# Kernel tuning notes

Measured on AMD Instinct MI355X. Metric: run time of the kernel, lower is better.

## Reference

```python
import jax, jax.numpy as jnp
import numpy as np
from jax import lax
from jax.scipy.special import logsumexp

N, M, K = 50000, 1024, 64          # points, nodes, points-per-patch
D_PT, D_NODE = 64, 256             # point / node feature dims
NUM_CORR = 256                     # coarse correspondences (OT batch)
FINE_TOPK = 3
CONF_TH = 0.05
OUT_CORR = 1024                    # fixed-size fine correspondence output
OT_ITERS = 100
NEG = -1e4                         # finite stand-in for -inf (grad-safe)
EPS = 1e-8


def setup_inputs() -> dict:
    key = jax.random.key(0)
    k = jax.random.split(key, 13)
    f = jnp.float32
    return {
        "src_points": jax.random.uniform(k[0], (N, 3), f) * 10.0,
        "tgt_points": jax.random.uniform(k[1], (N, 3), f) * 10.0,
        "src_point_feats": jax.random.normal(k[2], (N, D_PT), f),
        "tgt_point_feats": jax.random.normal(k[3], (N, D_PT), f),
        "src_node_feats": jax.random.normal(k[4], (M, D_NODE), f),
        "tgt_node_feats": jax.random.normal(k[5], (M, D_NODE), f),
        "src_node_xyz": jax.random.uniform(k[6], (M, 3), f) * 10.0,
        "tgt_node_xyz": jax.random.uniform(k[7], (M, 3), f) * 10.0,
        "coarse_w": jax.random.normal(k[8], (D_NODE, D_NODE), f) / np.sqrt(D_NODE),
        "coarse_b": jnp.zeros((D_NODE,), f),
        "fine_w": jax.random.normal(k[9], (D_NODE, D_PT), f) / np.sqrt(D_PT),
        "fine_b": jnp.zeros((D_NODE,), f),
        "alpha": jnp.ones((), f),
    }


def sq_dist(a, b):
    # squared pairwise distance via gram trick, (Na, Nb)
    return (jnp.sum(a * a, -1)[:, None] + jnp.sum(b * b, -1)[None, :]
            - 2.0 * a @ b.T)


def point_to_node_partition(points, nodes):
    d = sq_dist(points, nodes)                       # (N, M)
    p2n = jnp.argmin(d, axis=1)                      # nearest node per point
    m = nodes.shape[0]
    node_masks = jnp.zeros((m,), bool).at[p2n].set(True)
    match = p2n[:, None] == jnp.arange(m)[None, :]   # point assigned to node
    dm = jnp.where(match, d, 1e12)
    _, knn_idx = lax.top_k(-dm.T, K)                 # (M, K) nearest assigned pts
    knn_node = p2n[knn_idx]
    knn_masks = knn_node == jnp.arange(m)[:, None]
    knn_idx = jnp.where(knn_masks, knn_idx, points.shape[0])  # pad index = N
    return node_masks, knn_idx, knn_masks


def coarse_matching(tgt_feats, src_feats, tgt_masks, src_masks):
    # exp(-||.||^2) similarity + dual normalization (GeoTransformer style)
    scores = jnp.exp(-sq_dist(tgt_feats, src_feats))
    valid = tgt_masks[:, None] & src_masks[None, :]
    scores = jnp.where(valid, scores, 0.0)
    s = (scores / (scores.sum(1, keepdims=True) + EPS)) * \
        (scores / (scores.sum(0, keepdims=True) + EPS))
    vals, idx = lax.top_k(s.reshape(-1), NUM_CORR)
    tgt_idx = idx // src_feats.shape[0]
    src_idx = idx % src_feats.shape[0]
    return tgt_idx, src_idx, vals


def log_optimal_transport(scores, row_masks, col_masks, alpha):
    B, R, C = scores.shape
    pad_c = jnp.broadcast_to(alpha, (B, R, 1)).astype(scores.dtype)
    pad_r = jnp.broadcast_to(alpha, (B, 1, C + 1)).astype(scores.dtype)
    padded = jnp.concatenate([jnp.concatenate([scores, pad_c], 2), pad_r], 1)
    inv_r = jnp.concatenate([~row_masks, jnp.zeros((B, 1), bool)], 1)  # (B,R+1)
    inv_c = jnp.concatenate([~col_masks, jnp.zeros((B, 1), bool)], 1)  # (B,C+1)
    padded = jnp.where(inv_r[:, :, None] | inv_c[:, None, :], NEG, padded)
    nr = row_masks.sum(1).astype(scores.dtype)
    nc = col_masks.sum(1).astype(scores.dtype)
    norm = -jnp.log(nr + nc)
    log_mu = jnp.concatenate(
        [jnp.broadcast_to(norm[:, None], (B, R)), (jnp.log(nc) + norm)[:, None]], 1)
    log_mu = jnp.where(inv_r, NEG, log_mu)
    log_nu = jnp.concatenate(
        [jnp.broadcast_to(norm[:, None], (B, C)), (jnp.log(nr) + norm)[:, None]], 1)
    log_nu = jnp.where(inv_c, NEG, log_nu)

    def body(_, uv):
        u, v = uv
        u = log_mu - logsumexp(padded + v[:, None, :], axis=2)
        v = log_nu - logsumexp(padded + u[:, :, None], axis=1)
        return (u, v)

    u, v = lax.fori_loop(0, OT_ITERS, body,
                         (jnp.zeros_like(log_mu), jnp.zeros_like(log_nu)))
    return padded + u[:, :, None] + v[:, None, :] - norm[:, None, None]


def _topk_row_mask(s, k):
    # boolean mask: True where s is among top-k along the last axis
    idx = lax.top_k(s, k)[1]                          # (B, R, k)
    B, R, _ = s.shape
    b = jnp.arange(B)[:, None, None]
    r = jnp.arange(R)[None, :, None]
    return jnp.zeros(s.shape, bool).at[b, r, idx].set(True)


def fine_matching(tgt_knn_pts, src_knn_pts, tgt_masks, src_masks, ot_scores):
    s = jnp.exp(ot_scores[:, :K, :K])                 # drop dustbin
    mask = tgt_masks[:, :, None] & src_masks[:, None, :]
    rm = _topk_row_mask(s, FINE_TOPK)
    cm = jnp.swapaxes(_topk_row_mask(jnp.swapaxes(s, 1, 2), FINE_TOPK), 1, 2)
    corr = rm & cm & (s > CONF_TH) & mask             # mutual topk + threshold
    sm = jnp.where(corr, s, 0.0)
    vals, idx = lax.top_k(sm.reshape(-1), OUT_CORR)   # fixed-size extraction
    b = idx // (K * K)
    r = (idx // K) % K
    c = idx % K
    valid = vals > 0.0
    tp = jnp.where(valid[:, None], tgt_knn_pts[b, r], 0.0)
    sp = jnp.where(valid[:, None], src_knn_pts[b, c], 0.0)
    return tp, sp, jnp.where(valid, vals, 0.0)


def reference(src_points, tgt_points, src_point_feats, tgt_point_feats,
              src_node_feats, tgt_node_feats, src_node_xyz, tgt_node_xyz,
              coarse_w, coarse_b, fine_w, fine_b, alpha):
    def l2n(x):
        return x / jnp.linalg.norm(x, axis=1, keepdims=True)

    s_node_f = l2n(src_node_feats @ coarse_w.T + coarse_b)
    t_node_f = l2n(tgt_node_feats @ coarse_w.T + coarse_b)
    s_pt_f = src_point_feats @ fine_w.T + fine_b       # (N, 256)
    t_pt_f = tgt_point_feats @ fine_w.T + fine_b

    s_nm, s_knn_i, s_knn_m = point_to_node_partition(src_points, src_node_xyz)
    t_nm, t_knn_i, t_knn_m = point_to_node_partition(tgt_points, tgt_node_xyz)

    s_pad_pts = jnp.concatenate([src_points, jnp.zeros((1, 3), src_points.dtype)], 0)
    t_pad_pts = jnp.concatenate([tgt_points, jnp.zeros((1, 3), tgt_points.dtype)], 0)
    s_knn_pts = s_pad_pts[s_knn_i]                     # (M, K, 3)
    t_knn_pts = t_pad_pts[t_knn_i]

    # coarse matching is under no_grad in the original
    t_ci, s_ci, node_scores = coarse_matching(
        lax.stop_gradient(t_node_f), lax.stop_gradient(s_node_f), t_nm, s_nm)

    s_c_knn_i = s_knn_i[s_ci]; t_c_knn_i = t_knn_i[t_ci]     # (B, K)
    s_c_knn_m = s_knn_m[s_ci]; t_c_knn_m = t_knn_m[t_ci]
    s_c_knn_p = s_knn_pts[s_ci]; t_c_knn_p = t_knn_pts[t_ci]  # (B, K, 3)

    s_pad_f = jnp.concatenate([s_pt_f, jnp.zeros((1, D_NODE), s_pt_f.dtype)], 0)
    t_pad_f = jnp.concatenate([t_pt_f, jnp.zeros((1, D_NODE), t_pt_f.dtype)], 0)
    s_c_knn_f = s_pad_f[s_c_knn_i]                     # (B, K, 256)
    t_c_knn_f = t_pad_f[t_c_knn_i]

    ms = jnp.einsum('bnd,bmd->bnm', t_c_knn_f, s_c_knn_f) / jnp.sqrt(
        jnp.asarray(D_NODE, t_c_knn_f.dtype))
    ms = log_optimal_transport(ms, t_c_knn_m, s_c_knn_m, alpha)  # (B, K+1, K+1)

    tp, sp, cs = fine_matching(lax.stop_gradient(t_c_knn_p),
                               lax.stop_gradient(s_c_knn_p),
                               t_c_knn_m, s_c_knn_m, lax.stop_gradient(ms))
    return ms, tp, sp, cs
```

## Files before the change

kernel.cpp:

```cpp
#include <hip/hip_runtime.h>
#include <math.h>

#define NPTS 50000
#define MN 1024
#define KK 64
#define DPT 64
#define DN 256
#define BCORR 256
#define OUTC 1024
#define OTI 100
#define NEGV (-1e4f)
#define EPSV 1e-8f
#define CAPL 512
#define CCAP 16384
#define HBLK 256
#define RCH 2048

__global__ void zero_all_kernel(int* cnt_s, int* cnt_t, int* ci_t, int* ci_s,
                                float* tpout){
  int t=blockIdx.x*256+threadIdx.x;
  if (t<MN){ cnt_s[t]=0; cnt_t[t]=0; }
  if (t<BCORR){ ci_t[t]=0; ci_s[t]=0; }
  for (int i=t;i<OUTC*3*2+OUTC;i+=gridDim.x*256) tpout[i]=0.0f;
}

__device__ __forceinline__ float blockReduceSum256(float v, float* red){
  int t=threadIdx.x;
  red[t]=v; __syncthreads();
  #pragma unroll
  for (int s=128;s>0;s>>=1){ if(t<s) red[t]+=red[t+s]; __syncthreads(); }
  float r=red[0]; __syncthreads();
  return r;
}

__global__ __launch_bounds__(256) void node_feat_kernel(
    const float* __restrict__ xt, const float* __restrict__ xs_,
    const float* __restrict__ W, const float* __restrict__ bias,
    float* __restrict__ outt, float* __restrict__ outs,
    float* __restrict__ sqt, float* __restrict__ sqs){
  __shared__ float xs[DN];
  __shared__ float red[256];
  int m=blockIdx.x, i=threadIdx.x;
  const float* x=(m<MN)? xt:xs_;
  float* out=(m<MN)? outt:outs;
  float* sq=(m<MN)? sqt:sqs;
  int mm=(m<MN)? m:m-MN;
  xs[i]=x[mm*DN+i];
  __syncthreads();
  float acc=bias[i];
  const float* wr=W+(size_t)i*DN;
  for (int k=0;k<DN;k++) acc=fmaf(wr[k],xs[k],acc);
  float ssq=blockReduceSum256(acc*acc,red);
  float o=acc/sqrtf(ssq);
  out[mm*DN+i]=o;
  float s2=blockReduceSum256(o*o,red);
  if(i==0) sq[mm]=s2;
}

__global__ __launch_bounds__(256) void p2n_kernel(
    const float* __restrict__ pts_s, const float* __restrict__ nd_s, int* __restrict__ o_s,
    const float* __restrict__ pts_t, const float* __restrict__ nd_t, int* __restrict__ o_t,
    int pb){
  __shared__ __align__(16) float4 nd[MN];
  int which=blockIdx.x>=pb;
  const float* pts=which? pts_t:pts_s;
  const float* nodes=which? nd_t:nd_s;
  int* p2n=which? o_t:o_s;
  int blk=which? blockIdx.x-pb : blockIdx.x;
  for (int j=threadIdx.x;j<MN;j+=256){
    float a=nodes[j*3+0], b=nodes[j*3+1], c=nodes[j*3+2];
    nd[j]=make_float4(a,b,c,a*a+b*b+c*c);
  }
  __syncthreads();
  int id=blk*256+threadIdx.x;
  if (id>=NPTS) return;
  float px=pts[id*3+0], py=pts[id*3+1], pz=pts[id*3+2];
  float pp=px*px+py*py+pz*pz;
  float best=3.4e38f; int bi=0;
  for (int j=0;j<MN;j++){
    float4 n=nd[j];
    float d=pp+n.w-2.0f*(px*n.x+py*n.y+pz*n.z);
    if (d<best){best=d;bi=j;}
  }
  p2n[id]=bi;
}

__global__ __launch_bounds__(256) void scatter_kernel(
    const int* __restrict__ p_s, int* __restrict__ c_s, int* __restrict__ l_s,
    const int* __restrict__ p_t, int* __restrict__ c_t, int* __restrict__ l_t,
    int pb){
  int which=blockIdx.x>=pb;
  const int* p2n=which? p_t:p_s;
  int* cnt=which? c_t:c_s;
  int* list=which? l_t:l_s;
  int blk=which? blockIdx.x-pb : blockIdx.x;
  int id=blk*256+threadIdx.x;
  if (id>=NPTS) return;
  int n=p2n[id];
  int t=atomicAdd(&cnt[n],1);
  if (t<CAPL) list[(size_t)n*CAPL+t]=id;
}

__global__ __launch_bounds__(256) void knn_kernel(
    const float* __restrict__ pts_s, const float* __restrict__ nd_s,
    const int* __restrict__ c_s, const int* __restrict__ l_s, int* __restrict__ k_s,
    const float* __restrict__ pts_t, const float* __restrict__ nd_t,
    const int* __restrict__ c_t, const int* __restrict__ l_t, int* __restrict__ k_t){
  __shared__ float ds[CAPL];
  __shared__ int is[CAPL];
  int which=blockIdx.x>=MN;
  const float* pts=which? pts_t:pts_s;
  const float* nodes=which? nd_t:nd_s;
  const int* cnt=which? c_t:c_s;
  const int* list=which? l_t:l_s;
  int* knn=which? k_t:k_s;
  int m=which? blockIdx.x-MN : blockIdx.x;
  int c=cnt[m]; if (c>CAPL) c=CAPL;
  float ax=nodes[m*3+0], ay=nodes[m*3+1], az=nodes[m*3+2];
  float nn2=ax*ax+ay*ay+az*az;
  for (int e=threadIdx.x;e<c;e+=256){
    int p=list[(size_t)m*CAPL+e];
    float px=pts[p*3+0],py=pts[p*3+1],pz=pts[p*3+2];
    float pp=px*px+py*py+pz*pz;
    ds[e]=pp+nn2-2.0f*(px*ax+py*ay+pz*az);
    is[e]=p;
  }
  for (int k=threadIdx.x;k<KK;k+=256) knn[m*KK+k]=NPTS;
  __syncthreads();
  for (int e=threadIdx.x;e<c;e+=256){
    float d=ds[e]; int p=is[e]; int r=0;
    for (int j=0;j<c;j++){
      float dj=ds[j];
      r += (dj<d || (dj==d && is[j]<p)) ? 1 : 0;
    }
    if (r<KK) knn[m*KK+r]=p;
  }
}

__global__ __launch_bounds__(256) void coarse_score_kernel(
    const float* __restrict__ tf, const float* __restrict__ sf,
    const float* __restrict__ tt, const float* __restrict__ ssv,
    const int* __restrict__ cnt_t, const int* __restrict__ cnt_s, float* __restrict__ S){
  __shared__ float tas[64][64];
  __shared__ float sbs[64][64];
  __shared__ float tta[64], ssa[64], tva[64], sva[64];
  int bi=blockIdx.x>>4, bj=blockIdx.x&15;
  int t=threadIdx.x, r=t&63, kq=t>>6, tx=t&15, ty=t>>4;
  if (kq==0){ tta[r]=tt[bi*64+r]; tva[r]=(cnt_t[bi*64+r]>0)?1.f:0.f; }
  if (kq==1){ ssa[r]=ssv[bj*64+r]; sva[r]=(cnt_s[bj*64+r]>0)?1.f:0.f; }
  float acc[4][4]={};
  const float* ta=tf+((size_t)bi*64)*DN;
  const float* sa=sf+((size_t)bj*64)*DN;
  for (int kc=0;kc<DN;kc+=64){
    __syncthreads();
    const float* tr_=ta+(size_t)r*DN+kc+kq*16;
    const float* sr_=sa+(size_t)r*DN+kc+kq*16;
    #pragma unroll
    for (int j4=0;j4<4;j4++){
      float4 v=*(const float4*)(tr_+4*j4);
      tas[kq*16+4*j4+0][r]=v.x; tas[kq*16+4*j4+1][r]=v.y;
      tas[kq*16+4*j4+2][r]=v.z; tas[kq*16+4*j4+3][r]=v.w;
      float4 w=*(const float4*)(sr_+4*j4);
      sbs[kq*16+4*j4+0][r]=w.x; sbs[kq*16+4*j4+1][r]=w.y;
      sbs[kq*16+4*j4+2][r]=w.z; sbs[kq*16+4*j4+3][r]=w.w;
    }
    __syncthreads();
    #pragma unroll
    for (int kk=0;kk<64;kk++){
      float4 a4=*(const float4*)(&tas[kk][4*ty]);
      float4 b4=*(const float4*)(&sbs[kk][4*tx]);
      float av[4]={a4.x,a4.y,a4.z,a4.w};
      float bv[4]={b4.x,b4.y,b4.z,b4.w};
      #pragma unroll
      for (int i=0;i<4;i++)
        #pragma unroll
        for (int j=0;j<4;j++) acc[i][j]=fmaf(av[i],bv[j],acc[i][j]);
    }
  }
  __syncthreads();
  #pragma unroll
  for (int i=0;i<4;i++){
    int rr=4*ty+i;
    #pragma unroll
    for (int j=0;j<4;j++){
      int cc=4*tx+j;
      float d=tta[rr]+ssa[cc]-2.0f*acc[i][j];
      float v=expf(-d);
      S[(size_t)(bi*64+rr)*MN + bj*64+cc]=(tva[rr]>0.f && sva[cc]>0.f)? v:0.0f;
    }
  }
}

__global__ __launch_bounds__(256) void sums_kernel(
    const float* __restrict__ S, float* __restrict__ rs, float* __restrict__ cs){
  __shared__ float red[256];
  __shared__ float red2[16][17];
  if (blockIdx.x<MN){
    int i=blockIdx.x;
    float a=0;
    for (int j=threadIdx.x;j<MN;j+=256) a+=S[(size_t)i*MN+j];
    float r=blockReduceSum256(a,red);
    if (threadIdx.x==0) rs[i]=r;
  } else {
    int j0=(blockIdx.x-MN)*16;
    int tx=threadIdx.x&15, ty=threadIdx.x>>4;
    float a=0;
    for (int i=ty;i<MN;i+=16) a+=S[(size_t)i*MN + j0+tx];
    red2[ty][tx]=a; __syncthreads();
    if (ty==0){
      float s=0;
      #pragma unroll
      for (int q=0;q<16;q++) s+=red2[q][tx];
      cs[j0+tx]=s;
    }
  }
}
__global__ __launch_bounds__(256) void dualnorm_hist_kernel(
    float* __restrict__ S, const float* __restrict__ rs, const float* __restrict__ cs,
    unsigned* __restrict__ partial1){
  __shared__ unsigned lh[256];
  lh[threadIdx.x]=0u; __syncthreads();
  for (int idx=blockIdx.x*256+threadIdx.x; idx<MN*MN; idx+=gridDim.x*256){
    int i=idx>>10, j=idx&1023;
    float v=S[idx];
    v=(v/(rs[i]+EPSV))*(v/(cs[j]+EPSV));
    S[idx]=v;
    if (v>0.0f) atomicAdd(&lh[__float_as_uint(v)>>24],1u);
  }
  __syncthreads();
  partial1[blockIdx.x*256+threadIdx.x]=lh[threadIdx.x];
}

__device__ __forceinline__ int scan_top(const unsigned* h, int k, unsigned start,
                                        unsigned* outcum){
  unsigned cum=start;
  for (int b=255;b>=0;b--){
    if (cum+h[b] >= (unsigned)k){ *outcum=cum; return b; }
    cum+=h[b];
  }
  *outcum=cum;
  return -1;
}
__device__ __forceinline__ void sum_partials(const unsigned* __restrict__ p,
                                             unsigned* h, int t){
  unsigned a=0;
  for (int i=0;i<HBLK;i++) a+=p[(size_t)i*256+t];
  h[t]=a;
}

__global__ __launch_bounds__(256) void hist_fine_kernel(
    const float* __restrict__ arr, int n, int k,
    const unsigned* __restrict__ p1, unsigned* __restrict__ p2){
  __shared__ unsigned h[256];
  __shared__ unsigned lh[256];
  __shared__ unsigned cbS;
  int t=threadIdx.x;
  lh[t]=0u;
  sum_partials(p1,h,t);
  __syncthreads();
  if (t==0){
    unsigned ab; int cb=scan_top(h,k,0u,&ab);
    if (cb<0) cb=0;
    cbS=(unsigned)cb;
  }
  __syncthreads();
  unsigned CB=cbS;
  for (int i=blockIdx.x*256+t; i<n; i+=gridDim.x*256){
    float v=arr[i];
    unsigned b=__float_as_uint(v);
    if (v>0.0f && (b>>24)==CB) atomicAdd(&lh[(b>>16)&255u],1u);
  }
  __syncthreads();
  p2[blockIdx.x*256+t]=lh[t];
}
__global__ __launch_bounds__(256) void hist_fine2_kernel(
    const float* __restrict__ arr, int n, int k,
    const unsigned* __restrict__ p1, const unsigned* __restrict__ p2,
    unsigned* __restrict__ p3, unsigned* __restrict__ cnt){
  __shared__ unsigned h[256];
  __shared__ unsigned lh[256];
  __shared__ unsigned t16S;
  int t=threadIdx.x;
  if (blockIdx.x==0 && t==0) *cnt=0u;
  lh[t]=0u;
  sum_partials(p1,h,t);
  __syncthreads();
  __shared__ unsigned cbS, ab1S;
  if (t==0){
    unsigned ab; int cb=scan_top(h,k,0u,&ab);
    if (cb<0){ cb=0; ab=ab-h[0]; }
    cbS=(unsigned)cb; ab1S=ab;
  }
  __syncthreads();
  sum_partials(p2,h,t);
  __syncthreads();
  if (t==0){
    unsigned ab2; int sb=scan_top(h,k,ab1S,&ab2);
    if (sb<0) sb=0;
    t16S=cbS*256u+(unsigned)sb;
  }
  __syncthreads();
  unsigned T16=t16S;
  for (int i=blockIdx.x*256+t; i<n; i+=gridDim.x*256){
    float v=arr[i];
    unsigned b=__float_as_uint(v);
    if (v>0.0f && (b>>16)==T16) atomicAdd(&lh[(b>>8)&255u],1u);
  }
  __syncthreads();
  p3[blockIdx.x*256+t]=lh[t];
}
__global__ __launch_bounds__(256) void compact_kernel(
    const float* __restrict__ arr, int n, int k,
    const unsigned* __restrict__ p1, const unsigned* __restrict__ p2,
    const unsigned* __restrict__ p3,
    float* __restrict__ cv, int* __restrict__ ci, unsigned* __restrict__ cnt){
  __shared__ unsigned h[256];
  __shared__ unsigned cbS, ab1S, t16S, ab2S, t24S;
  int t=threadIdx.x;
  sum_partials(p1,h,t);
  __syncthreads();
  if (t==0){
    unsigned ab; int cb=scan_top(h,k,0u,&ab);
    if (cb<0){ cb=0; ab=ab-h[0]; }
    cbS=(unsigned)cb; ab1S=ab;
  }
  __syncthreads();
  sum_partials(p2,h,t);
  __syncthreads();
  if (t==0){
    unsigned ab2; int sb=scan_top(h,k,ab1S,&ab2);
    if (sb<0) sb=0;
    t16S=cbS*256u+(unsigned)sb; ab2S=ab2;
  }
  __syncthreads();
  sum_partials(p3,h,t);
  __syncthreads();
  if (t==0){
    unsigned ab3; int sb=scan_top(h,k,ab2S,&ab3);
    if (sb<0) sb=0;
    t24S=t16S*256u+(unsigned)sb;
  }
  __syncthreads();
  unsigned T=t24S;
  for (int i=blockIdx.x*256+t; i<n; i+=gridDim.x*256){
    float v=arr[i];
    if (v>0.0f && (__float_as_uint(v)>>8)>=T){
      unsigned p=atomicAdd(cnt,1u);
      if (p<CCAP){ cv[p]=v; ci[p]=i; }
    }
  }
}
__global__ __launch_bounds__(256) void rank_coarse_kernel(
    const float* __restrict__ cv, const int* __restrict__ ci, const unsigned* __restrict__ meta,
    int* __restrict__ ti, int* __restrict__ si){
  __shared__ __align__(16) float scv[RCH];
  __shared__ __align__(16) int sci[RCH];
  int c=(int)meta[1]; if (c>CCAP) c=CCAP;
  int t=blockIdx.x*256+threadIdx.x;
  bool act=(t<c);
  float v=0.0f; int idx=0;
  if (act){ v=cv[t]; idx=ci[t]; }
  int rk=0;
  for (int base=0;base<c;base+=RCH){
    int lim=min(RCH,c-base);
    __syncthreads();
    for (int j=threadIdx.x;j<lim;j+=256){ scv[j]=cv[base+j]; sci[j]=ci[base+j]; }
    __syncthreads();
    if (act){
      int j=0;
      for (;j+4<=lim;j+=4){
        float4 v4=*(const float4*)(scv+j);
        int4 i4=*(const int4*)(sci+j);
        rk += (v4.x>v||(v4.x==v&&i4.x<idx))?1:0;
        rk += (v4.y>v||(v4.y==v&&i4.y<idx))?1:0;
        rk += (v4.z>v||(v4.z==v&&i4.z<idx))?1:0;
        rk += (v4.w>v||(v4.w==v&&i4.w<idx))?1:0;
      }
      for (;j<lim;j++) rk += (scv[j]>v||(scv[j]==v&&sci[j]<idx))?1:0;
    }
  }
  if (act && rk<BCORR){ ti[rk]=idx/MN; si[rk]=idx%MN; }
}
__global__ __launch_bounds__(256) void rank_fine_kernel(
    const float* __restrict__ cv, const int* __restrict__ ci, const unsigned* __restrict__ meta,
    const int* __restrict__ sel_t, const int* __restrict__ sel_s,
    const float* __restrict__ tpts, const float* __restrict__ spts,
    float* __restrict__ tp, float* __restrict__ sp, float* __restrict__ cs){
  __shared__ __align__(16) float scv[RCH];
  __shared__ __align__(16) int sci[RCH];
  int c=(int)meta[1]; if (c>CCAP) c=CCAP;
  int t=blockIdx.x*256+threadIdx.x;
  bool act=(t<c);
  float v=0.0f; int idx=0;
  if (act){ v=cv[t]; idx=ci[t]; }
  int rk=0;
  for (int base=0;base<c;base+=RCH){
    int lim=min(RCH,c-base);
    __syncthreads();
    for (int j=threadIdx.x;j<lim;j+=256){ scv[j]=cv[base+j]; sci[j]=ci[base+j]; }
    __syncthreads();
    if (act){
      int j=0;
      for (;j+4<=lim;j+=4){
        float4 v4=*(const float4*)(scv+j);
        int4 i4=*(const int4*)(sci+j);
        rk += (v4.x>v||(v4.x==v&&i4.x<idx))?1:0;
        rk += (v4.y>v||(v4.y==v&&i4.y<idx))?1:0;
        rk += (v4.z>v||(v4.z==v&&i4.z<idx))?1:0;
        rk += (v4.w>v||(v4.w==v&&i4.w<idx))?1:0;
      }
      for (;j<lim;j++) rk += (scv[j]>v||(scv[j]==v&&sci[j]<idx))?1:0;
    }
  }
  if (act && rk<OUTC){
    int b=idx>>12, r=(idx>>6)&63, cc=idx&63;
    int tpi=sel_t[b*KK+r], spi=sel_s[b*KK+cc];
    float tx=0,ty=0,tz=0,sx=0,sy=0,sz=0;
    if (tpi<NPTS){ tx=tpts[tpi*3]; ty=tpts[tpi*3+1]; tz=tpts[tpi*3+2]; }
    if (spi<NPTS){ sx=spts[spi*3]; sy=spts[spi*3+1]; sz=spts[spi*3+2]; }
    tp[rk*3+0]=tx; tp[rk*3+1]=ty; tp[rk*3+2]=tz;
    sp[rk*3+0]=sx; sp[rk*3+1]=sy; sp[rk*3+2]=sz;
    cs[rk]=v;
  }
}

__global__ __launch_bounds__(256) void sel_feat_kernel(
    const int* __restrict__ ci_t, const int* __restrict__ knn_t, const float* __restrict__ ptf_t,
    const int* __restrict__ ci_s, const int* __restrict__ knn_s, const float* __restrict__ ptf_s,
    const float* __restrict__ W, const float* __restrict__ bias,
    float* __restrict__ out_t, float* __restrict__ out_s,
    int* __restrict__ sel_tO, int* __restrict__ sel_sO){
  __shared__ float Xs[64][64];
  __shared__ float Ws[64][64];
  __shared__ float pvf[64];
  int which=blockIdx.x>=1024;
  const int* cib=which? ci_s:ci_t;
  const int* knn=which? knn_s:knn_t;
  const float* ptf=which? ptf_s:ptf_t;
  float* out=which? out_s:out_t;
  int* sel=which? sel_sO:sel_tO;
  int blk=which? blockIdx.x-1024 : blockIdx.x;
  int bj=blk>>2, bo=blk&3;
  int t=threadIdx.x, r=t&63, kq=t>>6, tx=t&15, ty=t>>4;
  int p=knn[cib[bj]*KK+r];
  if (kq==0){
    pvf[r]=(p!=NPTS)?1.f:0.f;
    if (bo==0) sel[bj*KK+r]=p;
  }
  const float* xr=ptf+(size_t)p*DPT+kq*16;
  #pragma unroll
  for (int j4=0;j4<4;j4++){
    float4 v=(p==NPTS)? make_float4(0.f,0.f,0.f,0.f) : *(const float4*)(xr+4*j4);
    Xs[kq*16+4*j4+0][r]=v.x; Xs[kq*16+4*j4+1][r]=v.y;
    Xs[kq*16+4*j4+2][r]=v.z; Xs[kq*16+4*j4+3][r]=v.w;
  }
  const float* wr=W+(size_t)(bo*64+r)*DPT+kq*16;
  #pragma unroll
  for (int j4=0;j4<4;j4++){
    float4 w=*(const float4*)(wr+4*j4);
    Ws[kq*16+4*j4+0][r]=w.x; Ws[kq*16+4*j4+1][r]=w.y;
    Ws[kq*16+4*j4+2][r]=w.z; Ws[kq*16+4*j4+3][r]=w.w;
  }
  __syncthreads();
  float acc[4][4]={};
  #pragma unroll
  for (int kk=0;kk<64;kk++){
    float4 a4=*(const float4*)(&Xs[kk][4*ty]);
    float4 w4=*(const float4*)(&Ws[kk][4*tx]);
    float av[4]={a4.x,a4.y,a4.z,a4.w};
    float wv[4]={w4.x,w4.y,w4.z,w4.w};
    #pragma unroll
    for (int i=0;i<4;i++)
      #pragma unroll
      for (int j=0;j<4;j++) acc[i][j]=fmaf(av[i],wv[j],acc[i][j]);
  }
  #pragma unroll
  for (int i=0;i<4;i++){
    int rr=4*ty+i;
    #pragma unroll
    for (int j=0;j<4;j++){
      int oo=4*tx+j;
      float v=acc[i][j]+bias[bo*64+oo];
      out[(size_t)(bj*64+rr)*DN + bo*64+oo]= (pvf[rr]>0.f)? v : 0.0f;
    }
  }
}

__global__ __launch_bounds__(256) void pbuild_kernel(
    const float* __restrict__ ft, const float* __restrict__ fs,
    const int* __restrict__ sel_t, const int* __restrict__ sel_s,
    const float* __restrict__ alpha_p, float* __restrict__ P){
  __shared__ float tas[64][64];
  __shared__ float sbs[64][64];
  __shared__ float tmv[64], smv[64];
  int b=blockIdx.x, t=threadIdx.x;
  int r=t&63, kq=t>>6, tx=t&15, ty=t>>4;
  if (kq==0) tmv[r]=(sel_t[b*KK+r]!=NPTS)?1.f:0.f;
  if (kq==1) smv[r]=(sel_s[b*KK+r]!=NPTS)?1.f:0.f;
  float acc[4][4]={};
  const float* tb=ft+(size_t)b*KK*DN;
  const float* sb=fs+(size_t)b*KK*DN;
  for (int kc=0;kc<DN;kc+=64){
    __syncthreads();
    const float* tr_=tb+(size_t)r*DN+kc+kq*16;
    const float* sr_=sb+(size_t)r*DN+kc+kq*16;
    #pragma unroll
    for (int j4=0;j4<4;j4++){
      float4 v=*(const float4*)(tr_+4*j4);
      tas[kq*16+4*j4+0][r]=v.x; tas[kq*16+4*j4+1][r]=v.y;
      tas[kq*16+4*j4+2][r]=v.z; tas[kq*16+4*j4+3][r]=v.w;
      float4 w=*(const float4*)(sr_+4*j4);
      sbs[kq*16+4*j4+0][r]=w.x; sbs[kq*16+4*j4+1][r]=w.y;
      sbs[kq*16+4*j4+2][r]=w.z; sbs[kq*16+4*j4+3][r]=w.w;
    }
    __syncthreads();
    #pragma unroll
    for (int kk=0;kk<64;kk++){
      float4 a4=*(const float4*)(&tas[kk][4*ty]);
      float4 b4=*(const float4*)(&sbs[kk][4*tx]);
      float av[4]={a4.x,a4.y,a4.z,a4.w};
      float bv[4]={b4.x,b4.y,b4.z,b4.w};
      #pragma unroll
      for (int i=0;i<4;i++)
        #pragma unroll
        for (int j=0;j<4;j++) acc[i][j]=fmaf(av[i],bv[j],acc[i][j]);
    }
  }
  __syncthreads();
  float alpha=alpha_p[0];
  float* Pb=P+(size_t)b*65*65;
  #pragma unroll
  for (int i=0;i<4;i++){
    int rr=4*ty+i;
    bool tok=tmv[rr]>0.f;
    #pragma unroll
    for (int j=0;j<4;j++){
      int cc=4*tx+j;
      bool invm=(!tok)||(smv[cc]<=0.f);
      Pb[rr*65+cc]= invm ? NEGV : acc[i][j]*0.0625f;
    }
  }
  if (t<64){
    Pb[64*65+t]=(smv[t]<=0.f)? NEGV : alpha;
    Pb[t*65+64]=(tmv[t]<=0.f)? NEGV : alpha;
  }
  if (t==64) Pb[64*65+64]=alpha;
}

__global__ __launch_bounds__(256,1) void ot_kernel(
    float* __restrict__ P, const int* __restrict__ sel_t, const int* __restrict__ sel_s){
  __shared__ float Ps[4225];
  __shared__ __align__(16) float partU[4][72], partV[4][72];
  __shared__ __align__(16) float pu64[4], pusv[4], pv64[4], pvsv[4];
  __shared__ float ufs[65], vfs[65];
  int b=blockIdx.x, t=threadIdx.x, w=t>>6, l=t&63;
  float* Pg=P+(size_t)b*4225;
  for (int e=t;e<4225;e+=256) Ps[e]=Pg[e];
  bool rv=(sel_t[b*KK+l]!=NPTS);
  bool cv=(sel_s[b*KK+l]!=NPTS);
  int nr=(int)__popcll(__ballot(rv));
  int nc=(int)__popcll(__ballot(cv));
  float inv=1.0f/(float)(nr+nc);
  float nrm=-logf((float)(nr+nc));
  float mu_l=inv, nu_l=inv, mu64=(float)nc*inv, nu64=(float)nr*inv;
  bool anyInvR=(nr<KK), anyInvC=(nc<KK);
  __syncthreads();
  const int c0=16*w;
  float aQ[16], bQ[16], r64Q[16], c64Q[16];
  #pragma unroll
  for (int j=0;j<16;j++){
    aQ[j]  =expf(Ps[l*65+c0+j]);
    bQ[j]  =expf(Ps[(c0+j)*65+l]);
    r64Q[j]=expf(Ps[64*65+c0+j]);
    c64Q[j]=expf(Ps[(c0+j)*65+64]);
  }
  float a64=expf(Ps[l*65+64]);
  float b64v=expf(Ps[64*65+l]);
  float k6464=expf(Ps[4224]);
  float U_l, V_l=1.0f, U64, V64=1.0f;
  unsigned p1U=0,p1V=0,p1a=0,p1b=0, p2U=0,p2V=0,p2a=0,p2b=0;

  for (int it=0; it<OTI; ++it){
    float p0=0,p1f=0,p2f=0,p3=0, d0=0,d1=0,d2=0,d3=0, z0=0,z1=0,z2=0,z3=0;
    #pragma unroll
    for (int j4=0;j4<4;j4++){
      float v0=__int_as_float(__builtin_amdgcn_readlane(__float_as_int(V_l), c0+4*j4+0));
      float v1=__int_as_float(__builtin_amdgcn_readlane(__float_as_int(V_l), c0+4*j4+1));
      float v2=__int_as_float(__builtin_amdgcn_readlane(__float_as_int(V_l), c0+4*j4+2));
      float v3=__int_as_float(__builtin_amdgcn_readlane(__float_as_int(V_l), c0+4*j4+3));
      p0=fmaf(aQ[4*j4+0],v0,p0); p1f=fmaf(aQ[4*j4+1],v1,p1f);
      p2f=fmaf(aQ[4*j4+2],v2,p2f); p3=fmaf(aQ[4*j4+3],v3,p3);
      d0=fmaf(r64Q[4*j4+0],v0,d0); d1=fmaf(r64Q[4*j4+1],v1,d1);
      d2=fmaf(r64Q[4*j4+2],v2,d2); d3=fmaf(r64Q[4*j4+3],v3,d3);
      z0+=v0; z1+=v1; z2+=v2; z3+=v3;
    }
    partU[w][l]=(p0+p1f)+(p2f+p3);
    if (l==0){ pu64[w]=(d0+d1)+(d2+d3); pusv[w]=(z0+z1)+(z2+z3); }
    __syncthreads();
    {
      float s=partU[0][l]+partU[1][l]+partU[2][l]+partU[3][l];
      float4 d4=*(const float4*)pu64;
      float srow=s+a64*V64;
      float s64=(d4.x+d4.y)+(d4.z+d4.w)+k6464*V64;
      U64=mu64/s64;
      if (anyInvR){
        float4 z4=*(const float4*)pusv;
        float sv=(z4.x+z4.y)+(z4.z+z4.w)+V64;
        U_l = rv ? (mu_l/srow) : (1.0f/sv);
      } else U_l = mu_l/srow;
    }
    float q0=0,q1=0,q2=0,q3=0, e0=0,e1=0,e2=0,e3=0, y0=0,y1=0,y2=0,y3=0;
    #pragma unroll
    for (int j4=0;j4<4;j4++){
      float u0=__int_as_float(__builtin_amdgcn_readlane(__float_as_int(U_l), c0+4*j4+0));
      float u1=__int_as_float(__builtin_amdgcn_readlane(__float_as_int(U_l), c0+4*j4+1));
      float u2=__int_as_float(__builtin_amdgcn_readlane(__float_as_int(U_l), c0+4*j4+2));
      float u3=__int_as_float(__builtin_amdgcn_readlane(__float_as_int(U_l), c0+4*j4+3));
      q0=fmaf(bQ[4*j4+0],u0,q0); q1=fmaf(bQ[4*j4+1],u1,q1);
      q2=fmaf(bQ[4*j4+2],u2,q2); q3=fmaf(bQ[4*j4+3],u3,q3);
      e0=fmaf(c64Q[4*j4+0],u0,e0); e1=fmaf(c64Q[4*j4+1],u1,e1);
      e2=fmaf(c64Q[4*j4+2],u2,e2); e3=fmaf(c64Q[4*j4+3],u3,e3);
      y0+=u0; y1+=u1; y2+=u2; y3+=u3;
    }
    partV[w][l]=(q0+q1)+(q2+q3);
    if (l==0){ pv64[w]=(e0+e1)+(e2+e3); pvsv[w]=(y0+y1)+(y2+y3); }
    __syncthreads();
    {
      float sc=partV[0][l]+partV[1][l]+partV[2][l]+partV[3][l];
      float4 e4=*(const float4*)pv64;
      float scol=sc+b64v*U64;
      float s64v=(e4.x+e4.y)+(e4.z+e4.w)+k6464*U64;
      V64=nu64/s64v;
      if (anyInvC){
        float4 y4=*(const float4*)pvsv;
        float su=(y4.x+y4.y)+(y4.z+y4.w)+U64;
        V_l = cv ? (nu_l/scol) : (1.0f/su);
      } else V_l = nu_l/scol;
    }
    unsigned cU=__float_as_uint(U_l), cVb=__float_as_uint(V_l);
    unsigned ca=__float_as_uint(U64), cb2=__float_as_uint(V64);
    bool e1s=(it>=1)&&(cU==p1U)&&(cVb==p1V)&&(ca==p1a)&&(cb2==p1b);
    bool e2s=(it>=2)&&(cU==p2U)&&(cVb==p2V)&&(ca==p2a)&&(cb2==p2b);
    unsigned long long b1=__ballot(e1s);
    unsigned long long b2=__ballot(e2s);
    p2U=p1U; p2V=p1V; p2a=p1a; p2b=p1b;
    p1U=cU; p1V=cVb; p1a=ca; p1b=cb2;
    if (b1==~0ULL) break;
    if (b2==~0ULL && (((OTI-1-it)&1)==0)) break;
  }
  if (w==0){
    ufs[l]=logf(U_l); vfs[l]=logf(V_l);
    if (l==0){ ufs[64]=logf(U64); vfs[64]=logf(V64); }
  }
  __syncthreads();
  for (int e=t;e<4225;e+=256){
    int r=e/65, c=e-65*r;
    Pg[e]=Ps[e]+ufs[r]+vfs[c]-nrm;
  }
}

__global__ __launch_bounds__(256) void fineprep_kernel(
    const float* __restrict__ P, const int* __restrict__ sel_t, const int* __restrict__ sel_s,
    float* __restrict__ smout, unsigned* __restrict__ partial1){
  __shared__ float s[KK*KK];
  __shared__ unsigned long long rowm[KK], colm[KK];
  __shared__ int tmk[KK], smk[KK];
  __shared__ unsigned lh[256];
  int b=blockIdx.x, t=threadIdx.x;
  lh[t]=0u;
  const float* Pb=P+(size_t)b*65*65;
  for (int e=t;e<KK*KK;e+=256){
    int r=e>>6, c=e&63;
    s[e]=expf(Pb[r*65+c]);
  }
  if (t<KK){ tmk[t]=(sel_t[b*KK+t]!=NPTS); smk[t]=(sel_s[b*KK+t]!=NPTS); }
  __syncthreads();
  if (t<KK){
    float v1=-1,v2=-1,v3=-1; int i1=0,i2=0,i3=0;
    const float* row=s+t*KK;
    for (int c=0;c<KK;c++){ float v=row[c];
      if (v>v1){v3=v2;i3=i2;v2=v1;i2=i1;v1=v;i1=c;}
      else if (v>v2){v3=v2;i3=i2;v2=v;i2=c;}
      else if (v>v3){v3=v;i3=c;}
    }
    rowm[t]=(1ULL<<i1)|(1ULL<<i2)|(1ULL<<i3);
  } else if (t<2*KK){
    int c=t-KK;
    float v1=-1,v2=-1,v3=-1; int i1=0,i2=0,i3=0;
    for (int r=0;r<KK;r++){ float v=s[r*KK+c];
      if (v>v1){v3=v2;i3=i2;v2=v1;i2=i1;v1=v;i1=r;}
      else if (v>v2){v3=v2;i3=i2;v2=v;i2=r;}
      else if (v>v3){v3=v;i3=r;}
    }
    colm[c]=(1ULL<<i1)|(1ULL<<i2)|(1ULL<<i3);
  }
  __syncthreads();
  for (int e=t;e<KK*KK;e+=256){
    int r=e>>6, c=e&63;
    float v=s[e];
    bool keep = ((rowm[r]>>c)&1ULL) && ((colm[c]>>r)&1ULL) && (v>0.05f) && tmk[r] && smk[c];
    float o= keep? v : 0.0f;
    smout[(size_t)b*KK*KK+e]=o;
    if (o>0.0f) atomicAdd(&lh[__float_as_uint(o)>>24],1u);
  }
  __syncthreads();
  partial1[b*256+t]=lh[t];
}

extern "C" void kernel_launch(void* const* d_in, const int* in_sizes, int n_in,
                              void* d_out, int out_size, void* d_ws, size_t ws_size,
                              hipStream_t stream){
  const float* src_pts=(const float*)d_in[0];
  const float* tgt_pts=(const float*)d_in[1];
  const float* src_pf =(const float*)d_in[2];
  const float* tgt_pf =(const float*)d_in[3];
  const float* src_nf =(const float*)d_in[4];
  const float* tgt_nf =(const float*)d_in[5];
  const float* src_nx =(const float*)d_in[6];
  const float* tgt_nx =(const float*)d_in[7];
  const float* cw=(const float*)d_in[8];
  const float* cb=(const float*)d_in[9];
  const float* fw=(const float*)d_in[10];
  const float* fb=(const float*)d_in[11];
  const float* alpha=(const float*)d_in[12];

  char* ws=(char*)d_ws;
  size_t off=0;
  auto A=[&](size_t bytes)->char*{
    char* p=ws+off; off+=(bytes+255)&~(size_t)255; return p; };

  float* tf    =(float*)A((size_t)MN*DN*4);
  float* sfb   =(float*)A((size_t)MN*DN*4);
  float* tt    =(float*)A(MN*4);
  float* ssv   =(float*)A(MN*4);
  int*   p2n_s =(int*)A((size_t)NPTS*4);
  int*   p2n_t =(int*)A((size_t)NPTS*4);
  int*   cnt_s =(int*)A(MN*4);
  int*   cnt_t =(int*)A(MN*4);
  int*   list_s=(int*)A((size_t)MN*CAPL*4);
  int*   list_t=(int*)A((size_t)MN*CAPL*4);
  int*   knn_s =(int*)A((size_t)MN*KK*4);
  int*   knn_t =(int*)A((size_t)MN*KK*4);
  float* Smat  =(float*)A((size_t)MN*MN*4);
  unsigned* partial1=(unsigned*)A((size_t)HBLK*256*4);
  unsigned* partial2=(unsigned*)A((size_t)HBLK*256*4);
  unsigned* partial3=(unsigned*)A((size_t)HBLK*256*4);
  unsigned* meta=(unsigned*)A(256);
  float* cand_v=(float*)A((size_t)CCAP*4);
  int*   cand_i=(int*)A((size_t)CCAP*4);
  int*   ci_t  =(int*)A(BCORR*4);
  int*   ci_s  =(int*)A(BCORR*4);
  int*   sel_t =(int*)A((size_t)BCORR*KK*4);
  int*   sel_s =(int*)A((size_t)BCORR*KK*4);
  float* feat_t=(float*)A((size_t)BCORR*KK*DN*4);
  float* feat_s=(float*)A((size_t)BCORR*KK*DN*4);
  float* smf   =(float*)A((size_t)BCORR*KK*KK*4);
  float* rs    =(float*)A(MN*4);
  float* csum  =(float*)A(MN*4);

  float* out=(float*)d_out;
  float* msout=out;
  float* tpout=out+(size_t)BCORR*65*65;
  float* spout=tpout+(size_t)OUTC*3;
  float* csout=spout+(size_t)OUTC*3;

  const int PB=(NPTS+255)/256;

  zero_all_kernel<<<28,256,0,stream>>>(cnt_s,cnt_t,ci_t,ci_s,tpout);
  node_feat_kernel<<<2*MN,256,0,stream>>>(tgt_nf,src_nf,cw,cb,tf,sfb,tt,ssv);
  p2n_kernel<<<2*PB,256,0,stream>>>(src_pts,src_nx,p2n_s,tgt_pts,tgt_nx,p2n_t,PB);
  scatter_kernel<<<2*PB,256,0,stream>>>(p2n_s,cnt_s,list_s,p2n_t,cnt_t,list_t,PB);
  knn_kernel<<<2*MN,256,0,stream>>>(src_pts,src_nx,cnt_s,list_s,knn_s,
                                    tgt_pts,tgt_nx,cnt_t,list_t,knn_t);

  coarse_score_kernel<<<256,256,0,stream>>>(tf,sfb,tt,ssv,cnt_t,cnt_s,Smat);
  sums_kernel<<<MN+64,256,0,stream>>>(Smat,rs,csum);
  dualnorm_hist_kernel<<<HBLK,256,0,stream>>>(Smat,rs,csum,partial1);

  hist_fine_kernel<<<HBLK,256,0,stream>>>(Smat,MN*MN,BCORR,partial1,partial2);
  hist_fine2_kernel<<<HBLK,256,0,stream>>>(Smat,MN*MN,BCORR,partial1,partial2,partial3,meta+1);
  compact_kernel<<<256,256,0,stream>>>(Smat,MN*MN,BCORR,partial1,partial2,partial3,
                                       cand_v,cand_i,meta+1);
  rank_coarse_kernel<<<CCAP/256,256,0,stream>>>(cand_v,cand_i,meta,ci_t,ci_s);

  sel_feat_kernel<<<2048,256,0,stream>>>(ci_t,knn_t,tgt_pf, ci_s,knn_s,src_pf,
                                         fw,fb,feat_t,feat_s,sel_t,sel_s);

  pbuild_kernel<<<BCORR,256,0,stream>>>(feat_t,feat_s,sel_t,sel_s,alpha,msout);
  ot_kernel<<<BCORR,256,0,stream>>>(msout,sel_t,sel_s);

  fineprep_kernel<<<BCORR,256,0,stream>>>(msout,sel_t,sel_s,smf,partial1);
  hist_fine_kernel<<<HBLK,256,0,stream>>>(smf,BCORR*KK*KK,OUTC,partial1,partial2);
  hist_fine2_kernel<<<HBLK,256,0,stream>>>(smf,BCORR*KK*KK,OUTC,partial1,partial2,partial3,meta+1);
  compact_kernel<<<256,256,0,stream>>>(smf,BCORR*KK*KK,OUTC,partial1,partial2,partial3,
                                       cand_v,cand_i,meta+1);
  rank_fine_kernel<<<CCAP/256,256,0,stream>>>(cand_v,cand_i,meta,sel_t,sel_s,
                                              tgt_pts,src_pts,tpout,spout,csout);
}
```

Measured before the change: 583.7 us.

## Restructure Sinkhorn loop to per-row threads with LDS-broadcast scaling vectors

Each row and column of the 65x65 OT matrix, dustbin included, now gets one thread: lanes 0-15 of each wave plus one dustbin thread. That thread holds a full exp'd row and column in registers and reads the U/V vectors from shared memory as float4 broadcasts. This replaces the earlier scheme, where 16-column slices were spread across waves with readlane, partial sums were reduced through shared memory, and the dustbin was a separate path. The goal is fewer cross-wave reductions per iteration, at the cost of more serial FMAs per thread and fewer active lanes. The bitwise-convergence early exit is removed, so all 100 iterations always run.

```diff
diff --git a/kernel.cpp b/kernel.cpp
--- a/kernel.cpp
+++ b/kernel.cpp
@@ -550,8 +550,7 @@
 __global__ __launch_bounds__(256,1) void ot_kernel(
     float* __restrict__ P, const int* __restrict__ sel_t, const int* __restrict__ sel_s){
   __shared__ float Ps[4225];
-  __shared__ __align__(16) float partU[4][72], partV[4][72];
-  __shared__ __align__(16) float pu64[4], pusv[4], pv64[4], pvsv[4];
+  __shared__ __align__(16) float Us[68], Vs[68];
   __shared__ float ufs[65], vfs[65];
   int b=blockIdx.x, t=threadIdx.x, w=t>>6, l=t&63;
   float* Pg=P+(size_t)b*4225;
@@ -562,96 +561,63 @@
   int nc=(int)__popcll(__ballot(cv));
   float inv=1.0f/(float)(nr+nc);
   float nrm=-logf((float)(nr+nc));
-  float mu_l=inv, nu_l=inv, mu64=(float)nc*inv, nu64=(float)nr*inv;
-  bool anyInvR=(nr<KK), anyInvC=(nc<KK);
-  __syncthreads();
-  const int c0=16*w;
-  float aQ[16], bQ[16], r64Q[16], c64Q[16];
-  #pragma unroll
-  for (int j=0;j<16;j++){
-    aQ[j]  =expf(Ps[l*65+c0+j]);
-    bQ[j]  =expf(Ps[(c0+j)*65+l]);
-    r64Q[j]=expf(Ps[64*65+c0+j]);
-    c64Q[j]=expf(Ps[(c0+j)*65+64]);
-  }
-  float a64=expf(Ps[l*65+64]);
-  float b64v=expf(Ps[64*65+l]);
-  float k6464=expf(Ps[4224]);
-  float U_l, V_l=1.0f, U64, V64=1.0f;
-  unsigned p1U=0,p1V=0,p1a=0,p1b=0, p2U=0,p2V=0,p2a=0,p2b=0;
+  float mu64=(float)nc*inv, nu64=(float)nr*inv;
+  if (t<68){ Vs[t]=(t<65)?1.0f:0.0f; Us[t]=0.0f; }
+  __syncthreads();
+  bool isRow = (l<16);
+  bool isDust = (w==0 && l==16);
+  int myr = isRow ? (16*w+l) : 64;
+  bool myrv = isRow ? (sel_t[b*KK+myr]!=NPTS) : true;
+  bool mycv = isRow ? (sel_s[b*KK+myr]!=NPTS) : true;
+  float mymu = isDust ? mu64 : inv;
+  float mynu = isDust ? nu64 : inv;
+  float aQ[64], bQ[64], a64, b64;
+  if (isRow || isDust){
+    #pragma unroll
+    for (int c=0;c<64;c++){
+      aQ[c]=expf(Ps[myr*65+c]);
+      bQ[c]=expf(Ps[c*65+myr]);
+    }
+    a64=expf(Ps[myr*65+64]);
+    b64=expf(Ps[64*65+myr]);
+  }
+  __syncthreads();
 
   for (int it=0; it<OTI; ++it){
-    float p0=0,p1f=0,p2f=0,p3=0, d0=0,d1=0,d2=0,d3=0, z0=0,z1=0,z2=0,z3=0;
-    #pragma unroll
-    for (int j4=0;j4<4;j4++){
-      float v0=__int_as_float(__builtin_amdgcn_readlane(__float_as_int(V_l), c0+4*j4+0));
-      float v1=__int_as_float(__builtin_amdgcn_readlane(__float_as_int(V_l), c0+4*j4+1));
-      float v2=__int_as_float(__builtin_amdgcn_readlane(__float_as_int(V_l), c0+4*j4+2));
-      float v3=__int_as_float(__builtin_amdgcn_readlane(__float_as_int(V_l), c0+4*j4+3));
-      p0=fmaf(aQ[4*j4+0],v0,p0); p1f=fmaf(aQ[4*j4+1],v1,p1f);
-      p2f=fmaf(aQ[4*j4+2],v2,p2f); p3=fmaf(aQ[4*j4+3],v3,p3);
-      d0=fmaf(r64Q[4*j4+0],v0,d0); d1=fmaf(r64Q[4*j4+1],v1,d1);
-      d2=fmaf(r64Q[4*j4+2],v2,d2); d3=fmaf(r64Q[4*j4+3],v3,d3);
-      z0+=v0; z1+=v1; z2+=v2; z3+=v3;
-    }
-    partU[w][l]=(p0+p1f)+(p2f+p3);
-    if (l==0){ pu64[w]=(d0+d1)+(d2+d3); pusv[w]=(z0+z1)+(z2+z3); }
-    __syncthreads();
-    {
-      float s=partU[0][l]+partU[1][l]+partU[2][l]+partU[3][l];
-      float4 d4=*(const float4*)pu64;
-      float srow=s+a64*V64;
-      float s64=(d4.x+d4.y)+(d4.z+d4.w)+k6464*V64;
-      U64=mu64/s64;
-      if (anyInvR){
-        float4 z4=*(const float4*)pusv;
-        float sv=(z4.x+z4.y)+(z4.z+z4.w)+V64;
-        U_l = rv ? (mu_l/srow) : (1.0f/sv);
-      } else U_l = mu_l/srow;
-    }
-    float q0=0,q1=0,q2=0,q3=0, e0=0,e1=0,e2=0,e3=0, y0=0,y1=0,y2=0,y3=0;
-    #pragma unroll
-    for (int j4=0;j4<4;j4++){
-      float u0=__int_as_float(__builtin_amdgcn_readlane(__float_as_int(U_l), c0+4*j4+0));
-      float u1=__int_as_float(__builtin_amdgcn_readlane(__float_as_int(U_l), c0+4*j4+1));
-      float u2=__int_as_float(__builtin_amdgcn_readlane(__float_as_int(U_l), c0+4*j4+2));
-      float u3=__int_as_float(__builtin_amdgcn_readlane(__float_as_int(U_l), c0+4*j4+3));
-      q0=fmaf(bQ[4*j4+0],u0,q0); q1=fmaf(bQ[4*j4+1],u1,q1);
-      q2=fmaf(bQ[4*j4+2],u2,q2); q3=fmaf(bQ[4*j4+3],u3,q3);
-      e0=fmaf(c64Q[4*j4+0],u0,e0); e1=fmaf(c64Q[4*j4+1],u1,e1);
-      e2=fmaf(c64Q[4*j4+2],u2,e2); e3=fmaf(c64Q[4*j4+3],u3,e3);
-      y0+=u0; y1+=u1; y2+=u2; y3+=u3;
-    }
-    partV[w][l]=(q0+q1)+(q2+q3);
-    if (l==0){ pv64[w]=(e0+e1)+(e2+e3); pvsv[w]=(y0+y1)+(y2+y3); }
-    __syncthreads();
-    {
-      float sc=partV[0][l]+partV[1][l]+partV[2][l]+partV[3][l];
-      float4 e4=*(const float4*)pv64;
-      float scol=sc+b64v*U64;
-      float s64v=(e4.x+e4.y)+(e4.z+e4.w)+k6464*U64;
-      V64=nu64/s64v;
-      if (anyInvC){
-        float4 y4=*(const float4*)pvsv;
-        float su=(y4.x+y4.y)+(y4.z+y4.w)+U64;
-        V_l = cv ? (nu_l/scol) : (1.0f/su);
-      } else V_l = nu_l/scol;
-    }
-    unsigned cU=__float_as_uint(U_l), cVb=__float_as_uint(V_l);
-    unsigned ca=__float_as_uint(U64), cb2=__float_as_uint(V64);
-    bool e1s=(it>=1)&&(cU==p1U)&&(cVb==p1V)&&(ca==p1a)&&(cb2==p1b);
-    bool e2s=(it>=2)&&(cU==p2U)&&(cVb==p2V)&&(ca==p2a)&&(cb2==p2b);
-    unsigned long long b1=__ballot(e1s);
-    unsigned long long b2=__ballot(e2s);
-    p2U=p1U; p2V=p1V; p2a=p1a; p2b=p1b;
-    p1U=cU; p1V=cVb; p1a=ca; p1b=cb2;
-    if (b1==~0ULL) break;
-    if (b2==~0ULL && (((OTI-1-it)&1)==0)) break;
-  }
-  if (w==0){
-    ufs[l]=logf(U_l); vfs[l]=logf(V_l);
-    if (l==0){ ufs[64]=logf(U64); vfs[64]=logf(V64); }
-  }
+    if (isRow || isDust){
+      float s0=0,s1=0,s2=0,s3=0, z0=0,z1=0,z2=0,z3=0;
+      #pragma unroll
+      for (int c4=0;c4<16;c4++){
+        float4 vv=*(const float4*)(Vs+4*c4);
+        s0=fmaf(aQ[4*c4+0],vv.x,s0); s1=fmaf(aQ[4*c4+1],vv.y,s1);
+        s2=fmaf(aQ[4*c4+2],vv.z,s2); s3=fmaf(aQ[4*c4+3],vv.w,s3);
+        z0+=vv.x; z1+=vv.y; z2+=vv.z; z3+=vv.w;
+      }
+      float V64=Vs[64];
+      float srow=(s0+s1)+(s2+s3)+a64*V64;
+      float sv  =(z0+z1)+(z2+z3)+V64;
+      float u = myrv ? (mymu/srow) : (1.0f/sv);
+      Us[myr]=u;
+    }
+    __syncthreads();
+    if (isRow || isDust){
+      float s0=0,s1=0,s2=0,s3=0, y0=0,y1=0,y2=0,y3=0;
+      #pragma unroll
+      for (int r4=0;r4<16;r4++){
+        float4 uu=*(const float4*)(Us+4*r4);
+        s0=fmaf(bQ[4*r4+0],uu.x,s0); s1=fmaf(bQ[4*r4+1],uu.y,s1);
+        s2=fmaf(bQ[4*r4+2],uu.z,s2); s3=fmaf(bQ[4*r4+3],uu.w,s3);
+        y0+=uu.x; y1+=uu.y; y2+=uu.z; y3+=uu.w;
+      }
+      float U64=Us[64];
+      float scol=(s0+s1)+(s2+s3)+b64*U64;
+      float su  =(y0+y1)+(y2+y3)+U64;
+      float v = mycv ? (mynu/scol) : (1.0f/su);
+      Vs[myr]=v;
+    }
+    __syncthreads();
+  }
+  if (t<65){ ufs[t]=logf(Us[t]); vfs[t]=logf(Vs[t]); }
   __syncthreads();
   for (int e=t;e<4225;e+=256){
     int r=e/65, c=e-65*r;
```

Result: slower. 608.2 us (+4.2%).
